# Kernel optimization log

Measured on AMD Instinct MI355X. Metric: run time of the kernel, lower is better.

Reference implementation:

```python
import jax, jax.numpy as jnp
import numpy as np
from jax import lax

B, S, L, H, D_IN, W = 128, 64, 137, 128, 64, 256  # batch, segments, logsig_dim, hidden, input_dim, vf_width


def setup_inputs() -> dict:
    key = jax.random.key(0)
    ks = jax.random.split(key, 12)
    rn = lambda k, s, sc: jax.random.normal(k, s, dtype=jnp.float32) * sc
    return {
        "times": jnp.arange(S + 1, dtype=jnp.float32),
        "logsig": rn(ks[0], (B, S, L), 0.1),
        "initial": rn(ks[1], (B, D_IN), 1.0),
        "in_w": rn(ks[2], (D_IN, H), 0.12),
        "in_b": rn(ks[3], (H,), 0.05),
        "h1_w": rn(ks[4], (H, W), 0.09),
        "h1_b": rn(ks[5], (W,), 0.05),
        "h2_w": rn(ks[6], (W, W), 0.06),
        "h2_b": rn(ks[7], (W,), 0.05),
        "vo_w": rn(ks[8], (W, W), 0.06),
        "vo_b": rn(ks[9], (W,), 0.05),
        "ml_w": rn(ks[10], (W, H * (L - 1)), 0.02),
        "ml_b": rn(ks[11], (H * (L - 1),), 0.01),
    }


def reference(times, logsig, initial, in_w, in_b, h1_w, h1_b, h2_w, h2_b, vo_w, vo_b, ml_w, ml_b):
    intervals = times                 # [S+1]; forward requires times == registered intervals
    coeffs = logsig[:, :, 1:]         # [B, S, L-1] (first logsig channel dropped)
    h0 = initial @ in_w + in_b        # [B, H]

    def func(t, y):
        # searchsorted + clamp, exactly as in the torch module
        idx = jnp.clip(jnp.searchsorted(intervals, t, side='left'), 1, S)
        dt = intervals[idx] - intervals[idx - 1]
        coeff = jnp.take(coeffs, idx - 1, axis=1)        # [B, L-1]
        h = jax.nn.relu(y @ h1_w + h1_b)                 # vf MLP (vf_depth-1 = 2 hidden layers)
        h = jax.nn.relu(h @ h2_w + h2_b)
        h = jnp.tanh(h @ vo_w + vo_b)                    # final tanh activation
        vf = (h @ ml_w + ml_b).reshape(B, H, L - 1)      # [B, H, L-1]
        return jnp.einsum('bhd,bd->bh', vf, coeff) / dt  # [B, H]

    def step(y, n):
        # one fixed-size Heun (RK2) step from intervals[n] to intervals[n+1]
        t0, t1 = intervals[n], intervals[n + 1]
        dt = t1 - t0
        k1 = func(t0, y)
        k2 = func(t1, y + dt * k1)
        y1 = y + 0.5 * dt * (k1 + k2)
        return y1, y1

    _, ys = lax.scan(step, h0, jnp.arange(S))            # ys: [S, B, H]
    features = jnp.concatenate([h0[:, None, :], jnp.swapaxes(ys, 0, 1)], axis=1)  # [B, S+1, H]
    return features, features[:, -1]
```

## Files before the change

### kernel.cpp

```cpp
#include <hip/hip_runtime.h>
#include <hip/hip_bf16.h>


#define BB 128
#define SS 64
#define LL 137
#define HH 128
#define DIN 64
#define WW 256
#define DD 136
#define KP 160
#define NC 32768
#define OUT2_OFF ((size_t)BB*(SS+1)*HH)

typedef __hip_bfloat16 bf16;
typedef __attribute__((ext_vector_type(8))) short short8;
typedef __attribute__((ext_vector_type(4))) float f32x4;
typedef _Float16 h2t __attribute__((ext_vector_type(2)));

__device__ __forceinline__ bf16 f2bf(float x){ return __float2bfloat16(x); }

__device__ __forceinline__ float fdot2u(unsigned w, unsigned y, float acc){
#if __has_builtin(__builtin_amdgcn_fdot2)
  return __builtin_amdgcn_fdot2(__builtin_bit_cast(h2t, w),
                                __builtin_bit_cast(h2t, y), acc, false);
#else
  h2t a = __builtin_bit_cast(h2t, w), b2 = __builtin_bit_cast(h2t, y);
  return acc + (float)a[0]*(float)b2[0] + (float)a[1]*(float)b2[1];
#endif
}
__device__ __forceinline__ float dot8(uint4 w, uint4 y, float acc){
  acc = fdot2u(w.x, y.x, acc);
  acc = fdot2u(w.y, y.y, acc);
  acc = fdot2u(w.z, y.z, acc);
  acc = fdot2u(w.w, y.w, acc);
  return acc;
}

__device__ __forceinline__ float fast_tanh(float x){
  float e = __expf(2.f*x);
#if __has_builtin(__builtin_amdgcn_rcpf)
  float r = __builtin_amdgcn_rcpf(e + 1.f);
#else
  float r = 1.f/(e + 1.f);
#endif
  return 1.f - 2.f*r;
}

__global__ void prep_coeff(const float* __restrict__ logsig, bf16* __restrict__ cA){
  int m = blockIdx.x;
  int d = threadIdx.x;
  int a = m >> 7, b = m & 127;
  float v = 0.0f;
  if (d < DD) v = logsig[(size_t)(b*SS + a)*LL + 1 + d];
  int kk = d >> 5, q = (d >> 3) & 3, jj = d & 7;
  cA[(((size_t)(kk*4 + q))*8192 + m)*8 + jj] = f2bf(v);
}

__global__ void prep_btt(const float* __restrict__ mlw, bf16* __restrict__ btt){
  int c = blockIdx.x;
  int d = threadIdx.x;
  int w = ((c >> 10) << 3) | (c & 7);
  int h = (c >> 3) & 127;
  float v = 0.0f;
  if (d < DD) v = mlw[(size_t)w*(HH*DD) + h*DD + d];
  int kk = d >> 5, q = (d >> 3) & 3, jj = d & 7;
  btt[(((size_t)(kk*4 + q))*NC + c)*8 + jj] = f2bf(v);
}

__global__ void prep_packw(const float* __restrict__ src, uint4* __restrict__ dst){
  int c = blockIdx.x, j = threadIdx.x;
  union { _Float16 h[8]; uint4 v; } u;
  #pragma unroll
  for (int r = 0; r < 8; ++r) u.h[r] = (_Float16)src[(size_t)(c*8+r)*WW + j];
  dst[c*WW + j] = u.v;
}

__global__ void abias_kernel(const float* __restrict__ mlb, const float* __restrict__ logsig,
                             float* __restrict__ Abias){
  int a = blockIdx.x, b = blockIdx.y;
  int h = threadIdx.x;
  __shared__ float cf[DD];
  for (int d = h; d < DD; d += HH) cf[d] = logsig[(size_t)(b*SS + a)*LL + 1 + d];
  __syncthreads();
  float acc = 0.f;
  const float* mb = mlb + (size_t)h*DD;
  #pragma unroll 8
  for (int d = 0; d < DD; ++d) acc += cf[d] * mb[d];
  Abias[((size_t)a*BB + b)*HH + h] = acc;
}

__global__ __launch_bounds__(512) void agemm_kernel(const bf16* __restrict__ cA,
                                                    const bf16* __restrict__ btt,
                                                    _Float16* __restrict__ As, int mAbs0){
  __shared__ __align__(16) char smb[81920];
  short* sm = (short*)smb;
  int mt = blockIdx.x, nt = blockIdx.y;
  int t = threadIdx.x, lane = t & 63, wid = t >> 6;
  int mBlockAbs = mAbs0 + mt*128;
  int c0 = nt*128;
  int mW = (wid & 3)*32, cW = (wid >> 2)*64;
  const uint4* aK = (const uint4*)cA;
  const uint4* bK = (const uint4*)btt;

  uint4 va[5], vb[5];
  #pragma unroll
  for (int r = 0; r < 5; ++r){
    int lin = t + r*512;
    int kq = lin >> 7;
    int row = lin & 127;
    va[r] = aK[(size_t)kq*8192 + mBlockAbs + row];
    vb[r] = bK[(size_t)kq*NC + c0 + row];
  }
  #pragma unroll
  for (int r = 0; r < 5; ++r){
    int lin = t + r*512;
    *(uint4*)(smb + lin*16) = va[r];
    *(uint4*)(smb + 40960 + lin*16) = vb[r];
  }
  __syncthreads();

  f32x4 acc[2][4];
  #pragma unroll
  for (int i = 0; i < 2; ++i)
    #pragma unroll
    for (int j = 0; j < 4; ++j)
      acc[i][j] = (f32x4){0.f,0.f,0.f,0.f};

  const int mr = lane & 15, q = lane >> 4;
  #pragma unroll
  for (int kk = 0; kk < 5; ++kk){
    short8 af[2], bfr[4];
    #pragma unroll
    for (int mi = 0; mi < 2; ++mi)
      af[mi]  = *(const short8*)(smb + ((size_t)((kk*4+q)*128) + mW + mi*16 + mr)*16);
    #pragma unroll
    for (int ci = 0; ci < 4; ++ci)
      bfr[ci] = *(const short8*)(smb + 40960 + ((size_t)((kk*4+q)*128) + cW + ci*16 + mr)*16);
    #pragma unroll
    for (int mi = 0; mi < 2; ++mi)
      #pragma unroll
      for (int ci = 0; ci < 4; ++ci)
        acc[mi][ci] = __builtin_amdgcn_mfma_f32_16x16x32_bf16(af[mi], bfr[ci], acc[mi][ci], 0, 0, 0);
  }
  __syncthreads();

  #pragma unroll
  for (int mi = 0; mi < 2; ++mi)
    #pragma unroll
    for (int ci = 0; ci < 4; ++ci){
      int col = cW + ci*16 + mr;
      #pragma unroll
      for (int r = 0; r < 4; ++r){
        int row = mW + mi*16 + q*4 + r;
        _Float16 hv = (_Float16)acc[mi][ci][r];
        sm[row*136 + col] = *(short*)&hv;
      }
    }
  __syncthreads();
  int mLocBlock = mt*128;
  #pragma unroll
  for (int rep = 0; rep < 4; ++rep){
    int idx = t + rep*512;
    int row = idx >> 4, seg = idx & 15;
    uint4 v = *(const uint4*)&sm[row*136 + seg*8];
    *(uint4*)(As + (size_t)(mLocBlock + row)*NC + c0 + seg*8) = v;
  }
}

__device__ __forceinline__ float nrde_func(
    int b, int wave, int lane,
    const uint4 (&w1r)[4], const uint4 (&w2r)[8],
    const uint4* vo_sm,
    const _Float16* yh, _Float16* h1h, _Float16* h2h, _Float16* h3h,
    const float* bs1, const float* bs2, const float* bsv,
    const _Float16* __restrict__ As, const float* __restrict__ Abias,
    int aLoc, int aAbs, float inv_dtf)
{
  const int j  = (wave << 4) | (lane & 15);
  const int q  = lane >> 4;
  const int h  = (wave << 3) | (lane & 7);
  const int q8 = lane >> 3;

  uint4 ar[4];
  {
    const uint4* Ap = (const uint4*)(As + ((size_t)aLoc*BB + b)*NC);
    #pragma unroll
    for (int cc = 0; cc < 4; ++cc) ar[cc] = Ap[((q8 << 2) + cc)*HH + h];
  }
  float ab = Abias[((size_t)aAbs*BB + b)*HH + h];

  {
    const uint4* yp = (const uint4*)yh + (q << 2);
    float a0 = 0.f, a1 = 0.f;
    a0 = dot8(w1r[0], yp[0], a0); a1 = dot8(w1r[1], yp[1], a1);
    a0 = dot8(w1r[2], yp[2], a0); a1 = dot8(w1r[3], yp[3], a1);
    float acc = a0 + a1;
    acc += __shfl_xor(acc, 16);
    acc += __shfl_xor(acc, 32);
    if (q == 0){ float v = bs1[j] + acc; h1h[j] = (_Float16)(v > 0.f ? v : 0.f); }
  }
  __syncthreads();
  {
    const uint4* hp = (const uint4*)h1h + (q << 3);
    float a0 = 0.f, a1 = 0.f;
    #pragma unroll
    for (int cc = 0; cc < 8; cc += 2){
      a0 = dot8(w2r[cc],   hp[cc],   a0);
      a1 = dot8(w2r[cc+1], hp[cc+1], a1);
    }
    float acc = a0 + a1;
    acc += __shfl_xor(acc, 16);
    acc += __shfl_xor(acc, 32);
    if (q == 0){ float v = bs2[j] + acc; h2h[j] = (_Float16)(v > 0.f ? v : 0.f); }
  }
  __syncthreads();
  {
    const uint4* wp = vo_sm + (q << 3)*WW + j;
    const uint4* hp = (const uint4*)h2h + (q << 3);
    float a0 = 0.f, a1 = 0.f;
    #pragma unroll
    for (int cc = 0; cc < 8; cc += 2){
      a0 = dot8(wp[cc*WW],     hp[cc],   a0);
      a1 = dot8(wp[(cc+1)*WW], hp[cc+1], a1);
    }
    float acc = a0 + a1;
    acc += __shfl_xor(acc, 16);
    acc += __shfl_xor(acc, 32);
    if (q == 0) h3h[j] = (_Float16)fast_tanh(bsv[j] + acc);
  }
  __syncthreads();
  {
    const uint4* hp = (const uint4*)h3h + (q8 << 2);
    float a0 = 0.f, a1 = 0.f;
    a0 = dot8(ar[0], hp[0], a0); a1 = dot8(ar[1], hp[1], a1);
    a0 = dot8(ar[2], hp[2], a0); a1 = dot8(ar[3], hp[3], a1);
    float acc = a0 + a1;
    acc += __shfl_xor(acc, 8);
    acc += __shfl_xor(acc, 16);
    acc += __shfl_xor(acc, 32);
    return (acc + ab) * inv_dtf;
  }
}

__global__ __launch_bounds__(1024) void scan_kernel(
    const float* __restrict__ times, const float* __restrict__ initial,
    const float* __restrict__ in_w, const float* __restrict__ in_b,
    const float* __restrict__ h1_b, const float* __restrict__ h2_b,
    const float* __restrict__ vo_b,
    const uint4* __restrict__ wp1, const uint4* __restrict__ wp2,
    const uint4* __restrict__ wpv,
    const _Float16* __restrict__ As, const float* __restrict__ Abias,
    float* __restrict__ y_state, float* __restrict__ out,
    int s0, int s1, int aBase)
{
  __shared__ __align__(16) uint4 vo_sm[32*WW];
  __shared__ __align__(16) _Float16 yh[HH];
  __shared__ __align__(16) _Float16 h1h[WW];
  __shared__ __align__(16) _Float16 h2h[WW];
  __shared__ __align__(16) _Float16 h3h[WW];
  __shared__ float yv[HH];
  __shared__ float bs1[WW], bs2[WW], bsv[WW];

  const int b = blockIdx.x, t = threadIdx.x;
  const int wave = t >> 6, lane = t & 63;
  const int h = (wave << 3) | (lane & 7);
  const bool tail = (lane >> 3) == 0;
  const int j = (wave << 4) | (lane & 15);
  const int q = lane >> 4;

  for (int i = t; i < 32*WW; i += 1024) vo_sm[i] = wpv[i];
  if (t < WW){ bs1[t] = h1_b[t]; bs2[t] = h2_b[t]; bsv[t] = vo_b[t]; }

  uint4 w1r[4], w2r[8];
  {
    const uint4* wp = wp1 + (q << 2)*WW + j;
    #pragma unroll
    for (int cc = 0; cc < 4; ++cc) w1r[cc] = wp[cc*WW];
  }
  {
    const uint4* wp = wp2 + (q << 3)*WW + j;
    #pragma unroll
    for (int cc = 0; cc < 8; ++cc) w2r[cc] = wp[cc*WW];
  }

  if (s0 == 0){
    if (t < HH){
      float acc = in_b[t];
      for (int i = 0; i < DIN; ++i)
        acc += initial[b*DIN + i] * in_w[(size_t)i*HH + t];
      yv[t] = acc; yh[t] = (_Float16)acc;
      out[(size_t)b*(SS+1)*HH + t] = acc;
    }
  } else if (t < HH){
    float v = y_state[b*HH + t];
    yv[t] = v; yh[t] = (_Float16)v;
  }
  __syncthreads();

  for (int n = s0; n < s1; ++n){
    float t0v = times[n], t1v = times[n+1];
    float dt = t1v - t0v;
    int idx1 = (n >= 1) ? n : 1;
    float dtf1 = times[idx1] - times[idx1-1];
    int a1 = (n >= 1) ? (n-1) : 0;
    float k1 = nrde_func(b, wave, lane, w1r, w2r, vo_sm, yh, h1h, h2h, h3h,
                         bs1, bs2, bsv, As, Abias, a1 - aBase, a1, 1.f/dtf1);
    if (tail) yh[h] = (_Float16)(yv[h] + dt*k1);
    __syncthreads();
    float k2 = nrde_func(b, wave, lane, w1r, w2r, vo_sm, yh, h1h, h2h, h3h,
                         bs1, bs2, bsv, As, Abias, n - aBase, n, 1.f/dt);
    if (tail){
      float ynew = yv[h] + 0.5f*dt*(k1 + k2);
      yv[h] = ynew; yh[h] = (_Float16)ynew;
      out[((size_t)b*(SS+1) + (n+1))*HH + h] = ynew;
    }
    __syncthreads();
  }

  if (tail){
    y_state[b*HH + h] = yv[h];
    if (s1 == SS) out[OUT2_OFF + (size_t)b*HH + h] = yv[h];
  }
}

extern "C" void kernel_launch(void* const* d_in, const int* in_sizes, int n_in,
                              void* d_out, int out_size, void* d_ws, size_t ws_size,
                              hipStream_t stream)
{
  (void)in_sizes; (void)n_in; (void)out_size;
  const float* times   = (const float*)d_in[0];
  const float* logsig  = (const float*)d_in[1];
  const float* initial = (const float*)d_in[2];
  const float* in_w    = (const float*)d_in[3];
  const float* in_b    = (const float*)d_in[4];
  const float* h1_w    = (const float*)d_in[5];
  const float* h1_b    = (const float*)d_in[6];
  const float* h2_w    = (const float*)d_in[7];
  const float* h2_b    = (const float*)d_in[8];
  const float* vo_w    = (const float*)d_in[9];
  const float* vo_b    = (const float*)d_in[10];
  const float* ml_w    = (const float*)d_in[11];
  const float* ml_b    = (const float*)d_in[12];
  float* out = (float*)d_out;

  char* ws = (char*)d_ws;
  size_t off = 0;
  bf16* cA      = (bf16*)(ws + off); off += (size_t)8192*KP*2;
  bf16* btt     = (bf16*)(ws + off); off += (size_t)NC*KP*2;
  float* Abias  = (float*)(ws + off); off += (size_t)SS*BB*HH*4;
  float* y_state= (float*)(ws + off); off += (size_t)BB*HH*4;
  uint4* wp1    = (uint4*)(ws + off); off += (size_t)16*WW*16;
  uint4* wp2    = (uint4*)(ws + off); off += (size_t)32*WW*16;
  uint4* wpv    = (uint4*)(ws + off); off += (size_t)32*WW*16;
  _Float16* As  = (_Float16*)(ws + off);
  size_t perA = (size_t)BB*HH*WW*2;
  size_t avail = (ws_size > off) ? (ws_size - off) : 0;
  int C = (int)(avail / perA);
  if (C > SS) C = SS;
  if (C < 2) return;

  prep_coeff<<<8192, 160, 0, stream>>>(logsig, cA);
  prep_btt<<<NC, 160, 0, stream>>>(ml_w, btt);
  abias_kernel<<<dim3(SS, BB), HH, 0, stream>>>(ml_b, logsig, Abias);
  prep_packw<<<16, WW, 0, stream>>>(h1_w, wp1);
  prep_packw<<<32, WW, 0, stream>>>(h2_w, wp2);
  prep_packw<<<32, WW, 0, stream>>>(vo_w, wpv);

  int s = 0, aB = 0;
  while (s < SS){
    int cc = SS - aB; if (cc > C) cc = C;
    agemm_kernel<<<dim3(cc, 256), 512, 0, stream>>>(cA, btt, As, aB*BB);
    int sEnd = aB + cc; if (sEnd > SS) sEnd = SS;
    scan_kernel<<<BB, 1024, 0, stream>>>(times, initial, in_w, in_b,
        h1_b, h2_b, vo_b, wp1, wp2, wpv, As, Abias, y_state, out, s, sEnd, aB);
    s = sEnd;
    aB = sEnd - 1;
  }
}
```

Before: 641.9 us.

## Keep vo weights and biases in registers, prefetch both A tiles per step

Moves the vo_w weight slice and the three bias vectors out of shared memory into per-thread registers. Both Heun stages' A-matrix fragments and biases are now loaded at the top of each step, so the k2 loads overlap the k1 compute. This removes LDS traffic and the 128KB shared staging of vo weights, but raises register pressure: each of the 1024 threads now holds about 32 uint4 of weights, which risks spills. The launch bound is also given a minimum-blocks hint.

Result: slower. 1.399 ms (+118.0%).

```diff
diff --git a/kernel.cpp b/kernel.cpp
--- a/kernel.cpp
+++ b/kernel.cpp
@@ -169,26 +169,15 @@
 }
 
 __device__ __forceinline__ float nrde_func(
-    int b, int wave, int lane,
-    const uint4 (&w1r)[4], const uint4 (&w2r)[8],
-    const uint4* vo_sm,
+    int wave, int lane,
+    const uint4 (&w1r)[4], const uint4 (&w2r)[8], const uint4 (&vor)[8],
+    const uint4 (&ar)[4], float ab,
     const _Float16* yh, _Float16* h1h, _Float16* h2h, _Float16* h3h,
-    const float* bs1, const float* bs2, const float* bsv,
-    const _Float16* __restrict__ As, const float* __restrict__ Abias,
-    int aLoc, int aAbs, float inv_dtf)
+    float b1, float b2, float bv, float inv_dtf)
 {
   const int j  = (wave << 4) | (lane & 15);
   const int q  = lane >> 4;
-  const int h  = (wave << 3) | (lane & 7);
   const int q8 = lane >> 3;
-
-  uint4 ar[4];
-  {
-    const uint4* Ap = (const uint4*)(As + ((size_t)aLoc*BB + b)*NC);
-    #pragma unroll
-    for (int cc = 0; cc < 4; ++cc) ar[cc] = Ap[((q8 << 2) + cc)*HH + h];
-  }
-  float ab = Abias[((size_t)aAbs*BB + b)*HH + h];
 
   {
     const uint4* yp = (const uint4*)yh + (q << 2);
@@ -198,7 +187,7 @@
     float acc = a0 + a1;
     acc += __shfl_xor(acc, 16);
     acc += __shfl_xor(acc, 32);
-    if (q == 0){ float v = bs1[j] + acc; h1h[j] = (_Float16)(v > 0.f ? v : 0.f); }
+    if (q == 0){ float v = b1 + acc; h1h[j] = (_Float16)(v > 0.f ? v : 0.f); }
   }
   __syncthreads();
   {
@@ -212,22 +201,21 @@
     float acc = a0 + a1;
     acc += __shfl_xor(acc, 16);
     acc += __shfl_xor(acc, 32);
-    if (q == 0){ float v = bs2[j] + acc; h2h[j] = (_Float16)(v > 0.f ? v : 0.f); }
-  }
-  __syncthreads();
-  {
-    const uint4* wp = vo_sm + (q << 3)*WW + j;
+    if (q == 0){ float v = b2 + acc; h2h[j] = (_Float16)(v > 0.f ? v : 0.f); }
+  }
+  __syncthreads();
+  {
     const uint4* hp = (const uint4*)h2h + (q << 3);
     float a0 = 0.f, a1 = 0.f;
     #pragma unroll
     for (int cc = 0; cc < 8; cc += 2){
-      a0 = dot8(wp[cc*WW],     hp[cc],   a0);
-      a1 = dot8(wp[(cc+1)*WW], hp[cc+1], a1);
+      a0 = dot8(vor[cc],   hp[cc],   a0);
+      a1 = dot8(vor[cc+1], hp[cc+1], a1);
     }
     float acc = a0 + a1;
     acc += __shfl_xor(acc, 16);
     acc += __shfl_xor(acc, 32);
-    if (q == 0) h3h[j] = (_Float16)fast_tanh(bsv[j] + acc);
+    if (q == 0) h3h[j] = (_Float16)fast_tanh(bv + acc);
   }
   __syncthreads();
   {
@@ -243,7 +231,7 @@
   }
 }
 
-__global__ __launch_bounds__(1024) void scan_kernel(
+__global__ __launch_bounds__(1024, 4) void scan_kernel(
     const float* __restrict__ times, const float* __restrict__ initial,
     const float* __restrict__ in_w, const float* __restrict__ in_b,
     const float* __restrict__ h1_b, const float* __restrict__ h2_b,
@@ -254,13 +242,11 @@
     float* __restrict__ y_state, float* __restrict__ out,
     int s0, int s1, int aBase)
 {
-  __shared__ __align__(16) uint4 vo_sm[32*WW];
   __shared__ __align__(16) _Float16 yh[HH];
   __shared__ __align__(16) _Float16 h1h[WW];
   __shared__ __align__(16) _Float16 h2h[WW];
   __shared__ __align__(16) _Float16 h3h[WW];
   __shared__ float yv[HH];
-  __shared__ float bs1[WW], bs2[WW], bsv[WW];
 
   const int b = blockIdx.x, t = threadIdx.x;
   const int wave = t >> 6, lane = t & 63;
@@ -268,11 +254,9 @@
   const bool tail = (lane >> 3) == 0;
   const int j = (wave << 4) | (lane & 15);
   const int q = lane >> 4;
-
-  for (int i = t; i < 32*WW; i += 1024) vo_sm[i] = wpv[i];
-  if (t < WW){ bs1[t] = h1_b[t]; bs2[t] = h2_b[t]; bsv[t] = vo_b[t]; }
-
-  uint4 w1r[4], w2r[8];
+  const int q8 = lane >> 3;
+
+  uint4 w1r[4], w2r[8], vor[8];
   {
     const uint4* wp = wp1 + (q << 2)*WW + j;
     #pragma unroll
@@ -283,6 +267,12 @@
     #pragma unroll
     for (int cc = 0; cc < 8; ++cc) w2r[cc] = wp[cc*WW];
   }
+  {
+    const uint4* wp = wpv + (q << 3)*WW + j;
+    #pragma unroll
+    for (int cc = 0; cc < 8; ++cc) vor[cc] = wp[cc*WW];
+  }
+  const float b1 = h1_b[j], b2 = h2_b[j], bv = vo_b[j];
 
   if (s0 == 0){
     if (t < HH){
@@ -304,12 +294,25 @@
     int idx1 = (n >= 1) ? n : 1;
     float dtf1 = times[idx1] - times[idx1-1];
     int a1 = (n >= 1) ? (n-1) : 0;
-    float k1 = nrde_func(b, wave, lane, w1r, w2r, vo_sm, yh, h1h, h2h, h3h,
-                         bs1, bs2, bsv, As, Abias, a1 - aBase, a1, 1.f/dtf1);
+
+    uint4 ar1[4], ar2[4];
+    {
+      const uint4* Ap1 = (const uint4*)(As + ((size_t)(a1 - aBase)*BB + b)*NC);
+      const uint4* Ap2 = (const uint4*)(As + ((size_t)(n  - aBase)*BB + b)*NC);
+      #pragma unroll
+      for (int cc = 0; cc < 4; ++cc) ar1[cc] = Ap1[((q8 << 2) + cc)*HH + h];
+      #pragma unroll
+      for (int cc = 0; cc < 4; ++cc) ar2[cc] = Ap2[((q8 << 2) + cc)*HH + h];
+    }
+    float ab1 = Abias[((size_t)a1*BB + b)*HH + h];
+    float ab2 = Abias[((size_t)n *BB + b)*HH + h];
+
+    float k1 = nrde_func(wave, lane, w1r, w2r, vor, ar1, ab1,
+                         yh, h1h, h2h, h3h, b1, b2, bv, 1.f/dtf1);
     if (tail) yh[h] = (_Float16)(yv[h] + dt*k1);
     __syncthreads();
-    float k2 = nrde_func(b, wave, lane, w1r, w2r, vo_sm, yh, h1h, h2h, h3h,
-                         bs1, bs2, bsv, As, Abias, n - aBase, n, 1.f/dt);
+    float k2 = nrde_func(wave, lane, w1r, w2r, vor, ar2, ab2,
+                         yh, h1h, h2h, h3h, b1, b2, bv, 1.f/dt);
     if (tail){
       float ynew = yv[h] + 0.5f*dt*(k1 + k2);
       yv[h] = ynew; yh[h] = (_Float16)ynew;
```

## Use LDS-only barriers, reload MLP weights per call, widen dot accumulators

Applied to the files above, without the earlier changes.

Replaces __syncthreads with a custom barrier that waits only on LDS/scalar counters (lgkmcnt) instead of also draining global memory ops, so outstanding global loads and stores (output writes, A-matrix prefetch) can stay in flight across barriers. Moves the h1/h2 weight loads from kernel-scope registers into each nrde_func call, reloading them from global/L2 every evaluation to cut register pressure. Splits the 8-term dot products into four independent accumulators for more ILP. The risk is extra global traffic per step, and the weaker barrier relies on no global-memory dependency crossing it.

Result: slower. 1.051 ms (+63.7%).

```diff
diff --git a/kernel.cpp b/kernel.cpp
--- a/kernel.cpp
+++ b/kernel.cpp
@@ -19,6 +19,13 @@
 typedef _Float16 h2t __attribute__((ext_vector_type(2)));
 
 __device__ __forceinline__ bf16 f2bf(float x){ return __float2bfloat16(x); }
+
+__device__ __forceinline__ void bar_lds(){
+  __builtin_amdgcn_sched_barrier(0);
+  asm volatile("s_waitcnt lgkmcnt(0)" ::: "memory");
+  __builtin_amdgcn_s_barrier();
+  __builtin_amdgcn_sched_barrier(0);
+}
 
 __device__ __forceinline__ float fdot2u(unsigned w, unsigned y, float acc){
 #if __has_builtin(__builtin_amdgcn_fdot2)
@@ -170,7 +177,7 @@
 
 __device__ __forceinline__ float nrde_func(
     int b, int wave, int lane,
-    const uint4 (&w1r)[4], const uint4 (&w2r)[8],
+    const uint4* __restrict__ wp1, const uint4* __restrict__ wp2,
     const uint4* vo_sm,
     const _Float16* yh, _Float16* h1h, _Float16* h2h, _Float16* h3h,
     const float* bs1, const float* bs2, const float* bsv,
@@ -182,7 +189,17 @@
   const int h  = (wave << 3) | (lane & 7);
   const int q8 = lane >> 3;
 
-  uint4 ar[4];
+  uint4 w1r[4], w2r[8], ar[4];
+  {
+    const uint4* wp = wp1 + (q << 2)*WW + j;
+    #pragma unroll
+    for (int cc = 0; cc < 4; ++cc) w1r[cc] = wp[cc*WW];
+  }
+  {
+    const uint4* wp = wp2 + (q << 3)*WW + j;
+    #pragma unroll
+    for (int cc = 0; cc < 8; ++cc) w2r[cc] = wp[cc*WW];
+  }
   {
     const uint4* Ap = (const uint4*)(As + ((size_t)aLoc*BB + b)*NC);
     #pragma unroll
@@ -200,36 +217,34 @@
     acc += __shfl_xor(acc, 32);
     if (q == 0){ float v = bs1[j] + acc; h1h[j] = (_Float16)(v > 0.f ? v : 0.f); }
   }
-  __syncthreads();
+  bar_lds();
   {
     const uint4* hp = (const uint4*)h1h + (q << 3);
-    float a0 = 0.f, a1 = 0.f;
-    #pragma unroll
-    for (int cc = 0; cc < 8; cc += 2){
-      a0 = dot8(w2r[cc],   hp[cc],   a0);
-      a1 = dot8(w2r[cc+1], hp[cc+1], a1);
-    }
-    float acc = a0 + a1;
+    float a0 = 0.f, a1 = 0.f, a2 = 0.f, a3 = 0.f;
+    a0 = dot8(w2r[0], hp[0], a0); a1 = dot8(w2r[1], hp[1], a1);
+    a2 = dot8(w2r[2], hp[2], a2); a3 = dot8(w2r[3], hp[3], a3);
+    a0 = dot8(w2r[4], hp[4], a0); a1 = dot8(w2r[5], hp[5], a1);
+    a2 = dot8(w2r[6], hp[6], a2); a3 = dot8(w2r[7], hp[7], a3);
+    float acc = (a0 + a1) + (a2 + a3);
     acc += __shfl_xor(acc, 16);
     acc += __shfl_xor(acc, 32);
     if (q == 0){ float v = bs2[j] + acc; h2h[j] = (_Float16)(v > 0.f ? v : 0.f); }
   }
-  __syncthreads();
+  bar_lds();
   {
     const uint4* wp = vo_sm + (q << 3)*WW + j;
     const uint4* hp = (const uint4*)h2h + (q << 3);
-    float a0 = 0.f, a1 = 0.f;
-    #pragma unroll
-    for (int cc = 0; cc < 8; cc += 2){
-      a0 = dot8(wp[cc*WW],     hp[cc],   a0);
-      a1 = dot8(wp[(cc+1)*WW], hp[cc+1], a1);
-    }
-    float acc = a0 + a1;
+    float a0 = 0.f, a1 = 0.f, a2 = 0.f, a3 = 0.f;
+    a0 = dot8(wp[0*WW], hp[0], a0); a1 = dot8(wp[1*WW], hp[1], a1);
+    a2 = dot8(wp[2*WW], hp[2], a2); a3 = dot8(wp[3*WW], hp[3], a3);
+    a0 = dot8(wp[4*WW], hp[4], a0); a1 = dot8(wp[5*WW], hp[5], a1);
+    a2 = dot8(wp[6*WW], hp[6], a2); a3 = dot8(wp[7*WW], hp[7], a3);
+    float acc = (a0 + a1) + (a2 + a3);
     acc += __shfl_xor(acc, 16);
     acc += __shfl_xor(acc, 32);
     if (q == 0) h3h[j] = (_Float16)fast_tanh(bsv[j] + acc);
   }
-  __syncthreads();
+  bar_lds();
   {
     const uint4* hp = (const uint4*)h3h + (q8 << 2);
     float a0 = 0.f, a1 = 0.f;
@@ -266,23 +281,9 @@
   const int wave = t >> 6, lane = t & 63;
   const int h = (wave << 3) | (lane & 7);
   const bool tail = (lane >> 3) == 0;
-  const int j = (wave << 4) | (lane & 15);
-  const int q = lane >> 4;
 
   for (int i = t; i < 32*WW; i += 1024) vo_sm[i] = wpv[i];
   if (t < WW){ bs1[t] = h1_b[t]; bs2[t] = h2_b[t]; bsv[t] = vo_b[t]; }
-
-  uint4 w1r[4], w2r[8];
-  {
-    const uint4* wp = wp1 + (q << 2)*WW + j;
-    #pragma unroll
-    for (int cc = 0; cc < 4; ++cc) w1r[cc] = wp[cc*WW];
-  }
-  {
-    const uint4* wp = wp2 + (q << 3)*WW + j;
-    #pragma unroll
-    for (int cc = 0; cc < 8; ++cc) w2r[cc] = wp[cc*WW];
-  }
 
   if (s0 == 0){
     if (t < HH){
@@ -304,18 +305,18 @@
     int idx1 = (n >= 1) ? n : 1;
     float dtf1 = times[idx1] - times[idx1-1];
     int a1 = (n >= 1) ? (n-1) : 0;
-    float k1 = nrde_func(b, wave, lane, w1r, w2r, vo_sm, yh, h1h, h2h, h3h,
+    float k1 = nrde_func(b, wave, lane, wp1, wp2, vo_sm, yh, h1h, h2h, h3h,
                          bs1, bs2, bsv, As, Abias, a1 - aBase, a1, 1.f/dtf1);
     if (tail) yh[h] = (_Float16)(yv[h] + dt*k1);
-    __syncthreads();
-    float k2 = nrde_func(b, wave, lane, w1r, w2r, vo_sm, yh, h1h, h2h, h3h,
+    bar_lds();
+    float k2 = nrde_func(b, wave, lane, wp1, wp2, vo_sm, yh, h1h, h2h, h3h,
                          bs1, bs2, bsv, As, Abias, n - aBase, n, 1.f/dt);
     if (tail){
       float ynew = yv[h] + 0.5f*dt*(k1 + k2);
       yv[h] = ynew; yh[h] = (_Float16)ynew;
       out[((size_t)b*(SS+1) + (n+1))*HH + h] = ynew;
     }
-    __syncthreads();
+    bar_lds();
   }
 
   if (tail){
```

## Make A-GEMM blocks loop over M tiles reusing B tile, reload weights per call

Applied to the files above, without the earlier changes.

The A-GEMM grid becomes 256x2 persistent blocks, each holding its B (ml_w) tile in shared memory while looping over half the M tiles, with the next A tile prefetched into registers and a separate output staging buffer. This cuts redundant B loads and the launch of many small blocks, at the cost of much larger shared memory per block (lower occupancy) and fewer blocks overall. Separately, the scan kernel no longer keeps the h1/h2 weight fragments in registers across the loop; nrde_func reloads them from global memory on every call, which frees registers but adds repeated global/cache traffic on the serial critical path.

Result: slower. 696.5 us (+8.5%).

```diff
diff --git a/kernel.cpp b/kernel.cpp
--- a/kernel.cpp
+++ b/kernel.cpp
@@ -92,85 +92,110 @@
 
 __global__ __launch_bounds__(512) void agemm_kernel(const bf16* __restrict__ cA,
                                                     const bf16* __restrict__ btt,
-                                                    _Float16* __restrict__ As, int mAbs0){
-  __shared__ __align__(16) char smb[81920];
-  short* sm = (short*)smb;
-  int mt = blockIdx.x, nt = blockIdx.y;
+                                                    _Float16* __restrict__ As,
+                                                    int mAbs0, int cc){
+  __shared__ __align__(16) char smb[116736];
+  short* o_sm = (short*)(smb + 81920);
+  int nt = blockIdx.x, half = blockIdx.y;
   int t = threadIdx.x, lane = t & 63, wid = t >> 6;
-  int mBlockAbs = mAbs0 + mt*128;
   int c0 = nt*128;
-  int mW = (wid & 3)*32, cW = (wid >> 2)*64;
+  int mT = (cc + 1) >> 1;
+  int mtBeg = half*mT, mtEnd = mtBeg + mT; if (mtEnd > cc) mtEnd = cc;
+  if (mtBeg >= mtEnd) return;
   const uint4* aK = (const uint4*)cA;
   const uint4* bK = (const uint4*)btt;
-
-  uint4 va[5], vb[5];
-  #pragma unroll
-  for (int r = 0; r < 5; ++r){
-    int lin = t + r*512;
-    int kq = lin >> 7;
-    int row = lin & 127;
-    va[r] = aK[(size_t)kq*8192 + mBlockAbs + row];
-    vb[r] = bK[(size_t)kq*NC + c0 + row];
-  }
-  #pragma unroll
-  for (int r = 0; r < 5; ++r){
-    int lin = t + r*512;
-    *(uint4*)(smb + lin*16) = va[r];
-    *(uint4*)(smb + 40960 + lin*16) = vb[r];
-  }
-  __syncthreads();
-
-  f32x4 acc[2][4];
-  #pragma unroll
-  for (int i = 0; i < 2; ++i)
-    #pragma unroll
-    for (int j = 0; j < 4; ++j)
-      acc[i][j] = (f32x4){0.f,0.f,0.f,0.f};
-
   const int mr = lane & 15, q = lane >> 4;
-  #pragma unroll
-  for (int kk = 0; kk < 5; ++kk){
-    short8 af[2], bfr[4];
+  const int mW = (wid & 3)*32, cW = (wid >> 2)*64;
+
+  {
+    uint4 vb[5], va[5];
+    #pragma unroll
+    for (int r = 0; r < 5; ++r){
+      int lin = t + r*512;
+      int kq = lin >> 7, row = lin & 127;
+      vb[r] = bK[(size_t)kq*NC + c0 + row];
+      va[r] = aK[(size_t)kq*8192 + (mAbs0 + mtBeg*128) + row];
+    }
+    #pragma unroll
+    for (int r = 0; r < 5; ++r){
+      int lin = t + r*512;
+      *(uint4*)(smb + 40960 + lin*16) = vb[r];
+      *(uint4*)(smb + lin*16) = va[r];
+    }
+  }
+  __syncthreads();
+
+  for (int mt = mtBeg; mt < mtEnd; ++mt){
+    uint4 va[5];
+    const bool more = (mt + 1 < mtEnd);
+    if (more){
+      #pragma unroll
+      for (int r = 0; r < 5; ++r){
+        int lin = t + r*512;
+        int kq = lin >> 7, row = lin & 127;
+        va[r] = aK[(size_t)kq*8192 + (mAbs0 + (mt+1)*128) + row];
+      }
+    }
+
+    f32x4 acc[2][4];
+    #pragma unroll
+    for (int i = 0; i < 2; ++i)
+      #pragma unroll
+      for (int j = 0; j < 4; ++j)
+        acc[i][j] = (f32x4){0.f,0.f,0.f,0.f};
+
+    #pragma unroll
+    for (int kk = 0; kk < 5; ++kk){
+      short8 af[2], bfr[4];
+      #pragma unroll
+      for (int mi = 0; mi < 2; ++mi)
+        af[mi]  = *(const short8*)(smb + ((size_t)((kk*4+q)*128) + mW + mi*16 + mr)*16);
+      #pragma unroll
+      for (int ci = 0; ci < 4; ++ci)
+        bfr[ci] = *(const short8*)(smb + 40960 + ((size_t)((kk*4+q)*128) + cW + ci*16 + mr)*16);
+      #pragma unroll
+      for (int mi = 0; mi < 2; ++mi)
+        #pragma unroll
+        for (int ci = 0; ci < 4; ++ci)
+          acc[mi][ci] = __builtin_amdgcn_mfma_f32_16x16x32_bf16(af[mi], bfr[ci], acc[mi][ci], 0, 0, 0);
+    }
+    __syncthreads();
+
     #pragma unroll
     for (int mi = 0; mi < 2; ++mi)
-      af[mi]  = *(const short8*)(smb + ((size_t)((kk*4+q)*128) + mW + mi*16 + mr)*16);
-    #pragma unroll
-    for (int ci = 0; ci < 4; ++ci)
-      bfr[ci] = *(const short8*)(smb + 40960 + ((size_t)((kk*4+q)*128) + cW + ci*16 + mr)*16);
-    #pragma unroll
-    for (int mi = 0; mi < 2; ++mi)
-      #pragma unroll
-      for (int ci = 0; ci < 4; ++ci)
-        acc[mi][ci] = __builtin_amdgcn_mfma_f32_16x16x32_bf16(af[mi], bfr[ci], acc[mi][ci], 0, 0, 0);
-  }
-  __syncthreads();
-
-  #pragma unroll
-  for (int mi = 0; mi < 2; ++mi)
-    #pragma unroll
-    for (int ci = 0; ci < 4; ++ci){
-      int col = cW + ci*16 + mr;
-      #pragma unroll
-      for (int r = 0; r < 4; ++r){
-        int row = mW + mi*16 + q*4 + r;
-        _Float16 hv = (_Float16)acc[mi][ci][r];
-        sm[row*136 + col] = *(short*)&hv;
+      #pragma unroll
+      for (int ci = 0; ci < 4; ++ci){
+        int col = cW + ci*16 + mr;
+        #pragma unroll
+        for (int r = 0; r < 4; ++r){
+          int row = mW + mi*16 + q*4 + r;
+          _Float16 hv = (_Float16)acc[mi][ci][r];
+          o_sm[row*136 + col] = *(short*)&hv;
+        }
       }
-    }
-  __syncthreads();
-  int mLocBlock = mt*128;
-  #pragma unroll
-  for (int rep = 0; rep < 4; ++rep){
-    int idx = t + rep*512;
-    int row = idx >> 4, seg = idx & 15;
-    uint4 v = *(const uint4*)&sm[row*136 + seg*8];
-    *(uint4*)(As + (size_t)(mLocBlock + row)*NC + c0 + seg*8) = v;
+    if (more){
+      #pragma unroll
+      for (int r = 0; r < 5; ++r){
+        int lin = t + r*512;
+        *(uint4*)(smb + lin*16) = va[r];
+      }
+    }
+    __syncthreads();
+
+    int mLocBlock = mt*128;
+    #pragma unroll
+    for (int rep = 0; rep < 4; ++rep){
+      int idx = t + rep*512;
+      int row = idx >> 4, seg = idx & 15;
+      uint4 v = *(const uint4*)&o_sm[row*136 + seg*8];
+      *(uint4*)(As + (size_t)(mLocBlock + row)*NC + c0 + seg*8) = v;
+    }
   }
 }
 
 __device__ __forceinline__ float nrde_func(
     int b, int wave, int lane,
-    const uint4 (&w1r)[4], const uint4 (&w2r)[8],
+    const uint4* __restrict__ wp1, const uint4* __restrict__ wp2,
     const uint4* vo_sm,
     const _Float16* yh, _Float16* h1h, _Float16* h2h, _Float16* h3h,
     const float* bs1, const float* bs2, const float* bsv,
@@ -182,7 +207,17 @@
   const int h  = (wave << 3) | (lane & 7);
   const int q8 = lane >> 3;
 
-  uint4 ar[4];
+  uint4 w1r[4], w2r[8], ar[4];
+  {
+    const uint4* wp = wp1 + (q << 2)*WW + j;
+    #pragma unroll
+    for (int cc = 0; cc < 4; ++cc) w1r[cc] = wp[cc*WW];
+  }
+  {
+    const uint4* wp = wp2 + (q << 3)*WW + j;
+    #pragma unroll
+    for (int cc = 0; cc < 8; ++cc) w2r[cc] = wp[cc*WW];
+  }
   {
     const uint4* Ap = (const uint4*)(As + ((size_t)aLoc*BB + b)*NC);
     #pragma unroll
@@ -266,23 +301,9 @@
   const int wave = t >> 6, lane = t & 63;
   const int h = (wave << 3) | (lane & 7);
   const bool tail = (lane >> 3) == 0;
-  const int j = (wave << 4) | (lane & 15);
-  const int q = lane >> 4;
 
   for (int i = t; i < 32*WW; i += 1024) vo_sm[i] = wpv[i];
   if (t < WW){ bs1[t] = h1_b[t]; bs2[t] = h2_b[t]; bsv[t] = vo_b[t]; }
-
-  uint4 w1r[4], w2r[8];
-  {
-    const uint4* wp = wp1 + (q << 2)*WW + j;
-    #pragma unroll
-    for (int cc = 0; cc < 4; ++cc) w1r[cc] = wp[cc*WW];
-  }
-  {
-    const uint4* wp = wp2 + (q << 3)*WW + j;
-    #pragma unroll
-    for (int cc = 0; cc < 8; ++cc) w2r[cc] = wp[cc*WW];
-  }
 
   if (s0 == 0){
     if (t < HH){
@@ -304,11 +325,11 @@
     int idx1 = (n >= 1) ? n : 1;
     float dtf1 = times[idx1] - times[idx1-1];
     int a1 = (n >= 1) ? (n-1) : 0;
-    float k1 = nrde_func(b, wave, lane, w1r, w2r, vo_sm, yh, h1h, h2h, h3h,
+    float k1 = nrde_func(b, wave, lane, wp1, wp2, vo_sm, yh, h1h, h2h, h3h,
                          bs1, bs2, bsv, As, Abias, a1 - aBase, a1, 1.f/dtf1);
     if (tail) yh[h] = (_Float16)(yv[h] + dt*k1);
     __syncthreads();
-    float k2 = nrde_func(b, wave, lane, w1r, w2r, vo_sm, yh, h1h, h2h, h3h,
+    float k2 = nrde_func(b, wave, lane, wp1, wp2, vo_sm, yh, h1h, h2h, h3h,
                          bs1, bs2, bsv, As, Abias, n - aBase, n, 1.f/dt);
     if (tail){
       float ynew = yv[h] + 0.5f*dt*(k1 + k2);
@@ -370,7 +391,7 @@
   int s = 0, aB = 0;
   while (s < SS){
     int cc = SS - aB; if (cc > C) cc = C;
-    agemm_kernel<<<dim3(cc, 256), 512, 0, stream>>>(cA, btt, As, aB*BB);
+    agemm_kernel<<<dim3(256, 2), 512, 0, stream>>>(cA, btt, As, aB*128, cc);
     int sEnd = aB + cc; if (sEnd > SS) sEnd = SS;
     scan_kernel<<<BB, 1024, 0, stream>>>(times, initial, in_w, in_b,
         h1_b, h2_b, vo_b, wp1, wp2, wpv, As, Abias, y_state, out, s, sEnd, aB);
```
